# Performance work log

Measured on AMD Instinct MI355X. Metric: run time of the kernel, lower is better.

The kernel has to match this reference:

```python
import math
import jax, jax.numpy as jnp
import numpy as np

# ---- config (mirrors ModelConfig) ----
B, T = 2, 2048
N_EMBD, N_HEAD, N_KV = 2048, 16, 4
DH = N_EMBD // N_HEAD          # 128
G = N_HEAD // N_KV             # 4
ROPE_THETA = 1e6
YARN_FACTOR = 64.0
ORIG_MAX_POS = 4096
BETA_FAST, BETA_SLOW = 4.0, 1.0
MSCALE, MSCALE_ALL_DIM = 1.0, 0.0


def _yarn_get_mscale(scale, mscale=1.0):
    if scale <= 1.0:
        return 1.0
    return 0.1 * mscale * math.log(scale) + 1.0


def yarn_inv_freq_and_factor():
    dim = DH
    base = ROPE_THETA
    factor = YARN_FACTOR
    if MSCALE and MSCALE_ALL_DIM:
        attn_factor = _yarn_get_mscale(factor, MSCALE) / _yarn_get_mscale(factor, MSCALE_ALL_DIM)
    else:
        attn_factor = _yarn_get_mscale(factor)

    def corr_dim(num_rot):
        return dim * math.log(ORIG_MAX_POS / (num_rot * 2 * math.pi)) / (2 * math.log(base))

    low = max(math.floor(corr_dim(BETA_FAST)), 0.0)
    high = min(math.ceil(corr_dim(BETA_SLOW)), float(dim - 1))
    if low == high:
        high += 0.001
    half = dim // 2
    t = np.arange(half, dtype=np.float32)
    ramp = np.clip((t - low) / (high - low), 0.0, 1.0)  # linear ramp
    pos = np.arange(0, dim, 2, dtype=np.float32) / dim
    pos_freqs = base ** pos
    inv_extrap = 1.0 / pos_freqs
    inv_interp = 1.0 / (factor * pos_freqs)
    extrap_factor = 1.0 - ramp
    inv = inv_interp * (1.0 - extrap_factor) + inv_extrap * extrap_factor
    return jnp.asarray(inv, jnp.float32), float(attn_factor)


INV_FREQ, ATTN_FACTOR = yarn_inv_freq_and_factor()


def apply_rope_yarn(x, positions, inv_freq, attn_factor):
    # x: [B, T, H, Dh] interleaved RoPE, then scale by attn_factor
    x32 = x.astype(jnp.float32)
    angles = positions.astype(jnp.float32)[:, None] * inv_freq[None, :]  # [T, Dh/2]
    cos = angles[None, :, None, :]  # broadcast shapes
    cos, sin = jnp.cos(cos), jnp.sin(angles)[None, :, None, :]
    x_even = x32[..., 0::2]
    x_odd = x32[..., 1::2]
    out_even = x_even * cos - x_odd * sin
    out_odd = x_even * sin + x_odd * cos
    out = jnp.stack([out_even, out_odd], axis=-1).reshape(x.shape)
    return (out * attn_factor).astype(x.dtype)


def setup_inputs() -> dict:
    key = jax.random.key(0)
    k1, k2, k3 = jax.random.split(key, 3)
    x = jax.random.normal(k1, (B, T, N_EMBD), jnp.float32)
    w_qkv = jax.random.normal(k2, (N_EMBD, N_EMBD + 2 * N_KV * DH), jnp.float32) * (N_EMBD ** -0.5)
    w_o = jax.random.normal(k3, (N_EMBD, N_EMBD), jnp.float32) * (N_EMBD ** -0.5)
    return {"x": x, "w_qkv": w_qkv, "w_o": w_o}


def reference(x, w_qkv, w_o):
    qkv = x @ w_qkv  # [B, T, n_embd + 2*n_kv*dh]
    q_raw = qkv[:, :, :N_EMBD]
    k_raw = qkv[:, :, N_EMBD:N_EMBD + N_KV * DH]
    v_raw = qkv[:, :, N_EMBD + N_KV * DH:]
    q = q_raw.reshape(B, T, N_HEAD, DH)
    k = k_raw.reshape(B, T, N_KV, DH)
    v = v_raw.reshape(B, T, N_KV, DH)

    pos = jnp.arange(T, dtype=jnp.int32)
    q = apply_rope_yarn(q, pos, INV_FREQ, ATTN_FACTOR)
    k = apply_rope_yarn(k, pos, INV_FREQ, ATTN_FACTOR)

    q = q.reshape(B, T, N_KV, G, DH).transpose(0, 2, 3, 1, 4)  # [B, kv, g, T, Dh]
    k = k.transpose(0, 2, 1, 3)  # [B, kv, T, Dh]
    v = v.transpose(0, 2, 1, 3)  # [B, kv, T, Dh]

    scale = 1.0 / math.sqrt(DH)
    att = jnp.einsum('bkgtd,bksd->bkgts', q, k) * scale
    causal = jnp.tril(jnp.ones((T, T), bool))[None, None, None]
    att = jnp.where(causal, att, jnp.asarray(-1e9, att.dtype))
    w = jax.nn.softmax(att, axis=-1)
    y = jnp.einsum('bkgts,bksd->bkgtd', w, v)
    y = y.transpose(0, 3, 1, 2, 4).reshape(B, T, N_EMBD)
    return y @ w_o
```

## Files before the change

### kernel.cpp

```cpp
#include <hip/hip_runtime.h>
#include <hip/hip_bf16.h>
#include <math.h>

#define B_    2
#define T_    2048
#define CEMB  2048
#define NH    16
#define NKV   4
#define DHD   128
#define QKVD  3072

typedef unsigned short u16;
typedef unsigned int   u32;
typedef __attribute__((ext_vector_type(8))) short  short8;
typedef __attribute__((ext_vector_type(4))) float  floatx4;

static __device__ __forceinline__ u16 f2bf(float f){
    union{float f;u32 u;}x; x.f = f; u32 u = x.u;
    return (u16)((u + 0x7fffu + ((u >> 16) & 1u)) >> 16);
}
static __device__ __forceinline__ float lo2f(u32 w){ union{u32 u;float f;}x; x.u = w << 16; return x.f; }
static __device__ __forceinline__ float hi2f(u32 w){ union{u32 u;float f;}x; x.u = w & 0xffff0000u; return x.f; }

static __device__ __forceinline__ void async_cp16(const u16* g, u16* lds_wave_base) {
    __builtin_amdgcn_global_load_lds(
        (const __attribute__((address_space(1))) void*)g,
        (__attribute__((address_space(3))) void*)lds_wave_base, 16, 0, 0);
}

__global__ __launch_bounds__(256) void convert_kernel(const float* __restrict__ in,
                                                      u16* __restrict__ out, int n8)
{
    const int i = blockIdx.x * 256 + threadIdx.x;
    if (i >= n8) return;
    const float4* p = reinterpret_cast<const float4*>(in);
    float4 a = p[i * 2], b = p[i * 2 + 1];
    uint4 o;
    o.x = (u32)f2bf(a.x) | ((u32)f2bf(a.y) << 16);
    o.y = (u32)f2bf(a.z) | ((u32)f2bf(a.w) << 16);
    o.z = (u32)f2bf(b.x) | ((u32)f2bf(b.y) << 16);
    o.w = (u32)f2bf(b.z) | ((u32)f2bf(b.w) << 16);
    reinterpret_cast<uint4*>(out)[i] = o;
}

__global__ __launch_bounds__(256) void transpose_f32_bf16(const float* __restrict__ in,
                                                          u16* __restrict__ out,
                                                          int R, int Cn)
{
    __shared__ float tl[32][33];
    const int tx = threadIdx.x & 31, ty = threadIdx.x >> 5;
    const int c0 = blockIdx.x << 5, r0 = blockIdx.y << 5;
    #pragma unroll
    for (int i = 0; i < 4; ++i)
        tl[ty + i * 8][tx] = in[(size_t)(r0 + ty + i * 8) * Cn + c0 + tx];
    __syncthreads();
    #pragma unroll
    for (int i = 0; i < 4; ++i)
        out[(size_t)(c0 + ty + i * 8) * R + r0 + tx] = f2bf(tl[tx][ty + i * 8]);
}

__global__ __launch_bounds__(256) void vt_build_kernel(const u16* __restrict__ qkv,
                                                       u16* __restrict__ vt)
{
    __shared__ u16 tl[32][33];
    const int tx = threadIdx.x & 31, ty = threadIdx.x >> 5;
    const int t0 = blockIdx.x << 5, d0 = blockIdx.y << 5;
    const int b = blockIdx.z >> 2, kv = blockIdx.z & 3;
    #pragma unroll
    for (int i = 0; i < 4; ++i)
        tl[ty + i * 8][tx] =
            qkv[(size_t)(b * T_ + t0 + ty + i * 8) * QKVD + CEMB + NKV * DHD + kv * DHD + d0 + tx];
    __syncthreads();
    #pragma unroll
    for (int i = 0; i < 4; ++i)
        vt[(size_t)((b * NKV + kv) * DHD + d0 + ty + i * 8) * T_ + t0 + tx] = tl[tx][ty + i * 8];
}

template <bool F32OUT>
__global__ __launch_bounds__(256) void gemm_mfma_kernel(const u16* __restrict__ A,
                                                        const u16* __restrict__ BT,
                                                        void* __restrict__ Cv,
                                                        int M, int N, int K)
{
    __shared__ u16 As[128 * 32];
    __shared__ u16 Bs[128 * 32];
    const int tid  = threadIdx.x;
    const int lane = tid & 63;
    const int wv   = tid >> 6;
    const int n16  = lane & 15;
    const int quad = lane >> 4;
    const int wm   = wv >> 1, wn = wv & 1;
    const int row0 = blockIdx.y << 7;
    const int col0 = blockIdx.x << 7;

    floatx4 acc[4][4];
    #pragma unroll
    for (int i = 0; i < 4; ++i)
        #pragma unroll
        for (int j = 0; j < 4; ++j) acc[i][j] = (floatx4)0.0f;

    for (int k0 = 0; k0 < K; k0 += 32) {
        __syncthreads();
        #pragma unroll
        for (int it = 0; it < 2; ++it) {
            const int idx = it * 256 + tid;
            const int m = idx >> 2, k8 = (idx & 3) << 3;
            async_cp16(A  + (size_t)(row0 + m) * K + k0 + k8, &As[(it * 256 + wv * 64) * 8]);
            async_cp16(BT + (size_t)(col0 + m) * K + k0 + k8, &Bs[(it * 256 + wv * 64) * 8]);
        }
        __syncthreads();
        short8 af[4], bf[4];
        #pragma unroll
        for (int mt = 0; mt < 4; ++mt)
            af[mt] = *reinterpret_cast<const short8*>(&As[(wm * 64 + mt * 16 + n16) * 32 + quad * 8]);
        #pragma unroll
        for (int nt = 0; nt < 4; ++nt)
            bf[nt] = *reinterpret_cast<const short8*>(&Bs[(wn * 64 + nt * 16 + n16) * 32 + quad * 8]);
        #pragma unroll
        for (int mt = 0; mt < 4; ++mt)
            #pragma unroll
            for (int nt = 0; nt < 4; ++nt)
                acc[mt][nt] = __builtin_amdgcn_mfma_f32_16x16x32_bf16(af[mt], bf[nt], acc[mt][nt], 0, 0, 0);
    }
    #pragma unroll
    for (int mt = 0; mt < 4; ++mt) {
        #pragma unroll
        for (int r = 0; r < 4; ++r) {
            const int row = row0 + wm * 64 + mt * 16 + quad * 4 + r;
            if (F32OUT) {
                float* C = reinterpret_cast<float*>(Cv);
                #pragma unroll
                for (int nt = 0; nt < 4; ++nt)
                    C[(size_t)row * N + col0 + wn * 64 + nt * 16 + n16] = acc[mt][nt][r];
            } else {
                u16* C = reinterpret_cast<u16*>(Cv);
                #pragma unroll
                for (int nt = 0; nt < 4; ++nt)
                    C[(size_t)row * N + col0 + wn * 64 + nt * 16 + n16] = f2bf(acc[mt][nt][r]);
            }
        }
    }
}

__global__ __launch_bounds__(256) void rope_kernel(
    u16* __restrict__ qkv, const float attn_factor, const float low, const float high)
{
    const int total = B_ * T_ * (NH + NKV) * (DHD / 2);
    int idx = blockIdx.x * 256 + threadIdx.x;
    if (idx >= total) return;
    const int d = idx & 63;
    int r = idx >> 6;
    const int h = r % (NH + NKV);
    r /= (NH + NKV);
    const int t = r % T_;
    const int b = r / T_;
    const int off = (h < NH) ? (h * DHD) : (CEMB + (h - NH) * DHD);

    u32* p = reinterpret_cast<u32*>(qkv + (size_t)(b * T_ + t) * QKVD + off) + d;
    u32 w = *p;
    float xe = lo2f(w), xo = hi2f(w);

    float df   = (float)d;
    float ramp = (df - low) / (high - low);
    ramp = fminf(fmaxf(ramp, 0.0f), 1.0f);
    float pf     = expf((2.0f * df / 128.0f) * 13.815510557964274f);
    float inv_ex = 1.0f / pf;
    float inv    = inv_ex * ((1.0f / 64.0f) * ramp + (1.0f - ramp));
    float ang = (float)t * inv;
    float s = sinf(ang), c = cosf(ang);
    float oe = (xe * c - xo * s) * attn_factor;
    float oo = (xe * s + xo * c) * attn_factor;
    *p = (u32)f2bf(oe) | ((u32)f2bf(oo) << 16);
}

__global__ __launch_bounds__(256, 2) void attn_mfma_kernel(const u16* __restrict__ qkv,
                                                           const u16* __restrict__ vt,
                                                           u16* __restrict__ y)
{
    __shared__ __align__(16) u16 Ksd[2][64 * 128];
    __shared__ __align__(16) u16 Vtsd[2][128 * 64];
    __shared__ u16 Pl[4 * 16 * 72];

    const int tid  = threadIdx.x;
    const int lane = tid & 63;
    const int wv   = tid >> 6;
    const int n16  = lane & 15;
    const int quad = lane >> 4;
    const int nx   = blockIdx.x;
    const int bh   = blockIdx.y;
    const int b    = bh >> 4;
    const int h    = bh & 15;
    const int kh   = h >> 2;

    const float C1 = 0.08838834764831845f * 1.4426950408889634f;

    u16* plw = Pl + wv * 16 * 72;
    const u16* kbase = qkv + (size_t)(b * T_) * QKVD + CEMB + kh * DHD;
    const u16* vbase = vt + (size_t)((b * NKV + kh) * DHD) * T_;

    auto dma_k = [&](int j0, int buf) {
        #pragma unroll
        for (int it = 0; it < 4; ++it) {
            const int P   = it * 256 + tid;
            const int row = P >> 4;
            const int lc  = (P & 15) ^ (row & 15);
            async_cp16(kbase + (size_t)(j0 + row) * QKVD + (lc << 3),
                       &Ksd[buf][(it * 256 + wv * 64) * 8]);
        }
    };
    auto dma_v = [&](int j0, int buf) {
        #pragma unroll
        for (int it = 0; it < 4; ++it) {
            const int P   = it * 256 + tid;
            const int row = P >> 3;
            const int lc  = (P & 7) ^ (row & 7);
            async_cp16(vbase + (size_t)row * T_ + j0 + (lc << 3),
                       &Vtsd[buf][(it * 256 + wv * 64) * 8]);
        }
    };

    #pragma unroll
    for (int qt = 0; qt < 2; ++qt) {
        const int i0 = ((qt == 0) ? (31 - nx) : nx) << 6;

        const int qrow = i0 + wv * 16 + n16;
        const u16* qp = qkv + (size_t)(b * T_ + qrow) * QKVD + h * DHD;
        short8 qf[4];
        #pragma unroll
        for (int kk = 0; kk < 4; ++kk)
            qf[kk] = *reinterpret_cast<const short8*>(qp + kk * 32 + quad * 8);

        floatx4 oacc[8];
        #pragma unroll
        for (int i = 0; i < 8; ++i) oacc[i] = (floatx4)0.0f;
        float m_cur = -INFINITY, l_cur = 0.0f;

        __syncthreads();
        dma_k(0, 0);
        dma_v(0, 0);

        for (int j0 = 0; j0 <= i0; j0 += 64) {
            const int buf = (j0 >> 6) & 1;
            __syncthreads();
            if (j0 + 64 <= i0) {
                dma_k(j0 + 64, buf ^ 1);
                dma_v(j0 + 64, buf ^ 1);
            }
            const u16* kb = Ksd[buf];
            const u16* vb = Vtsd[buf];

            floatx4 st[4];
            #pragma unroll
            for (int t = 0; t < 4; ++t) st[t] = (floatx4)0.0f;
            #pragma unroll
            for (int t = 0; t < 4; ++t) {
                #pragma unroll
                for (int kk = 0; kk < 4; ++kk) {
                    short8 a = *reinterpret_cast<const short8*>(
                        &kb[(t * 16 + n16) * 128 + (((kk * 4 + quad) ^ n16) << 3)]);
                    st[t] = __builtin_amdgcn_mfma_f32_16x16x32_bf16(a, qf[kk], st[t], 0, 0, 0);
                }
            }

            const bool diag = (j0 + 63 > i0 + wv * 16);
            float mloc = m_cur;
            #pragma unroll
            for (int t = 0; t < 4; ++t) {
                #pragma unroll
                for (int r = 0; r < 4; ++r) {
                    float s = st[t][r];
                    if (diag) {
                        const int key = j0 + t * 16 + quad * 4 + r;
                        if (key > qrow) s = -INFINITY;
                    }
                    st[t][r] = s;
                    mloc = fmaxf(mloc, s);
                }
            }
            mloc = fmaxf(mloc, __shfl_xor(mloc, 16));
            mloc = fmaxf(mloc, __shfl_xor(mloc, 32));
            const float alpha = exp2f((m_cur - mloc) * C1);
            m_cur = mloc;

            float lsum = 0.0f;
            #pragma unroll
            for (int t = 0; t < 4; ++t) {
                float p0 = exp2f((st[t][0] - mloc) * C1);
                float p1 = exp2f((st[t][1] - mloc) * C1);
                float p2 = exp2f((st[t][2] - mloc) * C1);
                float p3 = exp2f((st[t][3] - mloc) * C1);
                lsum += (p0 + p1) + (p2 + p3);
                uint2 pk;
                pk.x = (u32)f2bf(p0) | ((u32)f2bf(p1) << 16);
                pk.y = (u32)f2bf(p2) | ((u32)f2bf(p3) << 16);
                *reinterpret_cast<uint2*>(&plw[n16 * 72 + t * 16 + quad * 4]) = pk;
            }
            lsum += __shfl_xor(lsum, 16);
            lsum += __shfl_xor(lsum, 32);
            l_cur = l_cur * alpha + lsum;

            #pragma unroll
            for (int dt = 0; dt < 8; ++dt) {
                oacc[dt][0] *= alpha; oacc[dt][1] *= alpha;
                oacc[dt][2] *= alpha; oacc[dt][3] *= alpha;
            }

            #pragma unroll
            for (int kt = 0; kt < 2; ++kt) {
                short8 pfrag = *reinterpret_cast<const short8*>(&plw[n16 * 72 + kt * 32 + quad * 8]);
                #pragma unroll
                for (int dt = 0; dt < 8; ++dt) {
                    short8 vfrag = *reinterpret_cast<const short8*>(
                        &vb[(dt * 16 + n16) * 64 + (((kt * 4 + quad) ^ (n16 & 7)) << 3)]);
                    oacc[dt] = __builtin_amdgcn_mfma_f32_16x16x32_bf16(vfrag, pfrag, oacc[dt], 0, 0, 0);
                }
            }
        }

        const float linv = 1.0f / l_cur;
        u16* yp = y + (size_t)(b * T_ + qrow) * CEMB + h * DHD + quad * 4;
        #pragma unroll
        for (int dt = 0; dt < 8; ++dt) {
            u32 w0 = (u32)f2bf(oacc[dt][0] * linv) | ((u32)f2bf(oacc[dt][1] * linv) << 16);
            u32 w1 = (u32)f2bf(oacc[dt][2] * linv) | ((u32)f2bf(oacc[dt][3] * linv) << 16);
            *reinterpret_cast<u32*>(yp + dt * 16)     = w0;
            *reinterpret_cast<u32*>(yp + dt * 16 + 2) = w1;
        }
    }
}

extern "C" void kernel_launch(void* const* d_in, const int* in_sizes, int n_in,
                              void* d_out, int out_size, void* d_ws, size_t ws_size,
                              hipStream_t stream) {
    const size_t NX   = (size_t)B_ * T_ * CEMB;
    const size_t NWQ  = (size_t)CEMB * QKVD;
    const size_t NWO  = (size_t)CEMB * CEMB;
    const size_t NQKV = (size_t)B_ * T_ * QKVD;
    const size_t NY   = NX;

    u16* qkv = (u16*)d_ws;
    u16* y   = qkv + NQKV;
    u16* xb  = y + NY;
    u16* wqT = xb + NX;
    u16* woT = wqT + NWQ;
    u16* vtb = xb;

    convert_kernel<<<(int)(NX / 8 + 255) / 256, 256, 0, stream>>>((const float*)d_in[0], xb, (int)(NX / 8));
    transpose_f32_bf16<<<dim3(QKVD / 32, CEMB / 32), 256, 0, stream>>>((const float*)d_in[1], wqT, CEMB, QKVD);
    transpose_f32_bf16<<<dim3(CEMB / 32, CEMB / 32), 256, 0, stream>>>((const float*)d_in[2], woT, CEMB, CEMB);

    gemm_mfma_kernel<false><<<dim3(QKVD / 128, (B_ * T_) / 128), 256, 0, stream>>>(
        xb, wqT, qkv, B_ * T_, QKVD, CEMB);

    const double two_pi = 6.283185307179586476925286766559;
    double corr4 = 128.0 * log(4096.0 / (4.0 * two_pi)) / (2.0 * log(1.0e6));
    double corr1 = 128.0 * log(4096.0 / (1.0 * two_pi)) / (2.0 * log(1.0e6));
    double lowd  = floor(corr4); if (lowd < 0.0) lowd = 0.0;
    double highd = ceil(corr1);  if (highd > 127.0) highd = 127.0;
    if (lowd == highd) highd += 0.001;
    float attn_factor = (float)(0.1 * log(64.0) + 1.0);

    const int rope_total = B_ * T_ * (NH + NKV) * (DHD / 2);
    rope_kernel<<<(rope_total + 255) / 256, 256, 0, stream>>>(
        qkv, attn_factor, (float)lowd, (float)highd);

    vt_build_kernel<<<dim3(T_ / 32, DHD / 32, B_ * NKV), 256, 0, stream>>>(qkv, vtb);

    attn_mfma_kernel<<<dim3(T_ / 128, B_ * NH), 256, 0, stream>>>(qkv, vtb, y);

    gemm_mfma_kernel<true><<<dim3(CEMB / 128, (B_ * T_) / 128), 256, 0, stream>>>(
        y, woT, d_out, B_ * T_, CEMB, CEMB);
}
```

Before: 337.1 us.

## Use lazy softmax rescaling, hardware bf16 pack, and MFMA priority hints in attention

The online-softmax update now rescales the output accumulator and running sum only when some row's new maximum exceeds the stored maximum by more than a threshold, set via a wave-wide vote. Otherwise the stale maximum is kept and the per-tile alpha multiplies are skipped. The software bf16 rounding is replaced with the v_cvt_pk_bf16_f32 instruction, the exponent argument is folded into an FMA, and s_setprio is raised around the MFMA blocks so waves issuing matrix work get priority. Skipping rescales lets exponentials grow up to 2^8 before renormalising, which trades some numeric headroom for fewer VALU ops in the inner loop.

Result: faster. 327.8 us (-2.8%).

```diff
diff --git a/kernel.cpp b/kernel.cpp
--- a/kernel.cpp
+++ b/kernel.cpp
@@ -21,6 +21,12 @@
 }
 static __device__ __forceinline__ float lo2f(u32 w){ union{u32 u;float f;}x; x.u = w << 16; return x.f; }
 static __device__ __forceinline__ float hi2f(u32 w){ union{u32 u;float f;}x; x.u = w & 0xffff0000u; return x.f; }
+
+static __device__ __forceinline__ u32 cvt_pk_bf16(float lo, float hi){
+    u32 r;
+    asm("v_cvt_pk_bf16_f32 %0, %1, %2" : "=v"(r) : "v"(lo), "v"(hi));
+    return r;
+}
 
 static __device__ __forceinline__ void async_cp16(const u16* g, u16* lds_wave_base) {
     __builtin_amdgcn_global_load_lds(
@@ -252,6 +258,7 @@
             floatx4 st[4];
             #pragma unroll
             for (int t = 0; t < 4; ++t) st[t] = (floatx4)0.0f;
+            __builtin_amdgcn_s_setprio(1);
             #pragma unroll
             for (int t = 0; t < 4; ++t) {
                 #pragma unroll
@@ -261,50 +268,56 @@
                     st[t] = __builtin_amdgcn_mfma_f32_16x16x32_bf16(a, qf[kk], st[t], 0, 0, 0);
                 }
             }
+            __builtin_amdgcn_s_setprio(0);
 
             const bool diag = (j0 + 63 > i0 + wv * 16);
-            float mloc = m_cur;
+            float tmax = -INFINITY;
             #pragma unroll
             for (int t = 0; t < 4; ++t) {
-                #pragma unroll
-                for (int r = 0; r < 4; ++r) {
-                    float s = st[t][r];
-                    if (diag) {
+                if (diag) {
+                    #pragma unroll
+                    for (int r = 0; r < 4; ++r) {
                         const int key = j0 + t * 16 + quad * 4 + r;
-                        if (key > qrow) s = -INFINITY;
+                        if (key > qrow) st[t][r] = -INFINITY;
                     }
-                    st[t][r] = s;
-                    mloc = fmaxf(mloc, s);
                 }
-            }
-            mloc = fmaxf(mloc, __shfl_xor(mloc, 16));
-            mloc = fmaxf(mloc, __shfl_xor(mloc, 32));
-            const float alpha = exp2f((m_cur - mloc) * C1);
-            m_cur = mloc;
-
+                tmax = fmaxf(tmax,
+                             fmaxf(fmaxf(st[t][0], st[t][1]), fmaxf(st[t][2], st[t][3])));
+            }
+            tmax = fmaxf(tmax, __shfl_xor(tmax, 16));
+            tmax = fmaxf(tmax, __shfl_xor(tmax, 32));
+
+            if (!__all((tmax - m_cur) * C1 <= 8.0f)) {
+                const float mnew  = fmaxf(m_cur, tmax);
+                const float alpha = exp2f((m_cur - mnew) * C1);
+                m_cur = mnew;
+                l_cur *= alpha;
+                #pragma unroll
+                for (int dt = 0; dt < 8; ++dt) {
+                    oacc[dt][0] *= alpha; oacc[dt][1] *= alpha;
+                    oacc[dt][2] *= alpha; oacc[dt][3] *= alpha;
+                }
+            }
+
+            const float mC = m_cur * C1;
             float lsum = 0.0f;
             #pragma unroll
             for (int t = 0; t < 4; ++t) {
-                float p0 = exp2f((st[t][0] - mloc) * C1);
-                float p1 = exp2f((st[t][1] - mloc) * C1);
-                float p2 = exp2f((st[t][2] - mloc) * C1);
-                float p3 = exp2f((st[t][3] - mloc) * C1);
+                float p0 = exp2f(fmaf(st[t][0], C1, -mC));
+                float p1 = exp2f(fmaf(st[t][1], C1, -mC));
+                float p2 = exp2f(fmaf(st[t][2], C1, -mC));
+                float p3 = exp2f(fmaf(st[t][3], C1, -mC));
                 lsum += (p0 + p1) + (p2 + p3);
                 uint2 pk;
-                pk.x = (u32)f2bf(p0) | ((u32)f2bf(p1) << 16);
-                pk.y = (u32)f2bf(p2) | ((u32)f2bf(p3) << 16);
+                pk.x = cvt_pk_bf16(p0, p1);
+                pk.y = cvt_pk_bf16(p2, p3);
                 *reinterpret_cast<uint2*>(&plw[n16 * 72 + t * 16 + quad * 4]) = pk;
             }
             lsum += __shfl_xor(lsum, 16);
             lsum += __shfl_xor(lsum, 32);
-            l_cur = l_cur * alpha + lsum;
-
-            #pragma unroll
-            for (int dt = 0; dt < 8; ++dt) {
-                oacc[dt][0] *= alpha; oacc[dt][1] *= alpha;
-                oacc[dt][2] *= alpha; oacc[dt][3] *= alpha;
-            }
-
+            l_cur += lsum;
+
+            __builtin_amdgcn_s_setprio(1);
             #pragma unroll
             for (int kt = 0; kt < 2; ++kt) {
                 short8 pfrag = *reinterpret_cast<const short8*>(&plw[n16 * 72 + kt * 32 + quad * 8]);
@@ -315,14 +328,17 @@
                     oacc[dt] = __builtin_amdgcn_mfma_f32_16x16x32_bf16(vfrag, pfrag, oacc[dt], 0, 0, 0);
                 }
             }
+            __builtin_amdgcn_s_setprio(0);
         }
 
         const float linv = 1.0f / l_cur;
         u16* yp = y + (size_t)(b * T_ + qrow) * CEMB + h * DHD + quad * 4;
         #pragma unroll
         for (int dt = 0; dt < 8; ++dt) {
-            u32 w0 = (u32)f2bf(oacc[dt][0] * linv) | ((u32)f2bf(oacc[dt][1] * linv) << 16);
-            u32 w1 = (u32)f2bf(oacc[dt][2] * linv) | ((u32)f2bf(oacc[dt][3] * linv) << 16);
+            float a0 = oacc[dt][0] * linv, a1 = oacc[dt][1] * linv;
+            float a2 = oacc[dt][2] * linv, a3 = oacc[dt][3] * linv;
+            u32 w0 = cvt_pk_bf16(a0, a1);
+            u32 w1 = cvt_pk_bf16(a2, a3);
             *reinterpret_cast<u32*>(yp + dt * 16)     = w0;
             *reinterpret_cast<u32*>(yp + dt * 16 + 2) = w1;
         }
```
